# Performance work log

Hardware: AMD Instinct MI355X
Metric: run time of the kernel (lower is better)

## Reference

```python
import jax, jax.numpy as jnp
import numpy as np

ENC, STR_H, CELL_H, ATTN = 512, 256, 512, 512
B, L = 64, 1024


def setup_inputs() -> dict:
    key = jax.random.key(0)
    ks = jax.random.split(key, 12)
    s = lambda fan_in: 1.0 / np.sqrt(fan_in)
    return {
        "encoded_features_map": jax.random.normal(ks[0], (B, L, ENC), jnp.float32),
        "structural_hidden_state": jax.random.normal(ks[1], (1, B, STR_H), jnp.float32),
        "cell_content_hidden_state": jax.random.normal(ks[2], (1, B, CELL_H), jnp.float32),
        "W_enc": jax.random.uniform(ks[3], (ENC, ATTN), jnp.float32, -s(ENC), s(ENC)),
        "b_enc": jax.random.uniform(ks[4], (ATTN,), jnp.float32, -s(ENC), s(ENC)),
        "W_str": jax.random.uniform(ks[5], (STR_H, ATTN), jnp.float32, -s(STR_H), s(STR_H)),
        "b_str": jax.random.uniform(ks[6], (ATTN,), jnp.float32, -s(STR_H), s(STR_H)),
        "W_cell": jax.random.uniform(ks[7], (CELL_H, ATTN), jnp.float32, -s(CELL_H), s(CELL_H)),
        "b_cell": jax.random.uniform(ks[8], (ATTN,), jnp.float32, -s(CELL_H), s(CELL_H)),
        "W_comb": jax.random.uniform(ks[9], (ATTN, 1), jnp.float32, -s(ATTN), s(ATTN)),
        "b_comb": jax.random.uniform(ks[10], (1,), jnp.float32, -s(ATTN), s(ATTN)),
    }


def reference(encoded_features_map, structural_hidden_state, cell_content_hidden_state,
              W_enc, b_enc, W_str, b_str, W_cell, b_cell, W_comb, b_comb):
    # [B, L, A] projection of encoder features
    a_enc = jnp.einsum("ble,ea->bla", encoded_features_map, W_enc) + b_enc
    # [B, A] projections of the two hidden states (squeeze layer dim)
    a_str = structural_hidden_state[0] @ W_str + b_str
    a_cell = cell_content_hidden_state[0] @ W_cell + b_cell
    # broadcast add + ReLU + scalar score: [B, L]
    h = jax.nn.relu(a_enc + a_str[:, None, :] + a_cell[:, None, :])
    scores = jnp.einsum("bla,ao->bl", h, W_comb) + b_comb[0]
    weights = jax.nn.softmax(scores, axis=1)  # over sequence dim
    # weighted sum over L -> [B, ENC]
    context = jnp.einsum("bl,ble->be", weights, encoded_features_map)
    return context
```

## Files before the change

### kernel.cpp

```cpp
#include <hip/hip_runtime.h>
#include <stdint.h>

#define ENC_D 512
#define ATTN_D 512
#define STR_D 256
#define CELL_D 512
#define BATCH 64
#define SEQ 1024
#define NROWS (BATCH * SEQ)

typedef __bf16 bf16x8 __attribute__((ext_vector_type(8)));
typedef float f32x4 __attribute__((ext_vector_type(4)));

__device__ __forceinline__ unsigned short f2bf(float f) {
    unsigned int u = __float_as_uint(f);
    u += 0x7fffu + ((u >> 16) & 1u);
    return (unsigned short)(u >> 16);
}

__device__ __forceinline__ void lds_cp16(void* l, const void* g) {
    __builtin_amdgcn_global_load_lds(
        (const __attribute__((address_space(1))) unsigned int*)g,
        (__attribute__((address_space(3))) unsigned int*)l, 16, 0, 0);
}

__global__ __launch_bounds__(256) void k_prep_wt(const float* __restrict__ W,
                                                 unsigned short* __restrict__ WF) {
    __shared__ unsigned short T[64 * 68];
    const int t = threadIdx.x;
    const int ei = blockIdx.x >> 3, ni = blockIdx.x & 7;
    const int e0 = ei * 64, n0 = ni * 64;

#pragma unroll
    for (int i = 0; i < 4; ++i) {
        const int idx = t + i * 256;
        const int r = idx >> 4, c4 = idx & 15;
        const float4 v = *(const float4*)(W + (size_t)(e0 + r) * ATTN_D + n0 + c4 * 4);
        T[(c4 * 4 + 0) * 68 + r] = f2bf(v.x);
        T[(c4 * 4 + 1) * 68 + r] = f2bf(v.y);
        T[(c4 * 4 + 2) * 68 + r] = f2bf(v.z);
        T[(c4 * 4 + 3) * 68 + r] = f2bf(v.w);
    }
    __syncthreads();

#pragma unroll
    for (int i = 0; i < 2; ++i) {
        const int q = t + i * 256;
        const int n = q >> 3, ge = q & 7;
        union { unsigned short s[8]; uint4 u; } o;
#pragma unroll
        for (int j = 0; j < 8; ++j) o.s[j] = T[n * 68 + ge * 8 + j];
        const int ng = n0 + n;
        const int g = ei * 8 + ge;
        const int nt = ng >> 4, c = ng & 15;
        const int ks = g >> 2, quad = g & 3;
        const int gi = nt * 1024 + ks * 64 + quad * 16 + c;
        *(uint4*)(WF + (size_t)gi * 8) = o.u;
    }
}

__global__ __launch_bounds__(128) void k_bias_part(const float* __restrict__ str,
                                                   const float* __restrict__ cell,
                                                   const float* __restrict__ Wstr,
                                                   const float* __restrict__ Wcell,
                                                   float* __restrict__ part) {
    __shared__ float sj[64];
    const int jq = blockIdx.x, b = blockIdx.y, t = threadIdx.x;
    const float* hvec;
    const float* Wrow;
    if (jq < 4) { hvec = str + b * STR_D + jq * 64;            Wrow = Wstr + (size_t)(jq * 64) * ATTN_D; }
    else        { hvec = cell + b * CELL_D + (jq - 4) * 64;    Wrow = Wcell + (size_t)((jq - 4) * 64) * ATTN_D; }
    if (t < 64) sj[t] = hvec[t];
    __syncthreads();

    f32x4 acc = {0.f, 0.f, 0.f, 0.f};
#pragma unroll 8
    for (int i = 0; i < 64; ++i) {
        const float s = sj[i];
        const float4 wv = *(const float4*)(Wrow + (size_t)i * ATTN_D + t * 4);
        acc[0] += s * wv.x; acc[1] += s * wv.y; acc[2] += s * wv.z; acc[3] += s * wv.w;
    }
    *(f32x4*)(part + (size_t)(jq * BATCH + b) * ATTN_D + t * 4) = acc;
}

__global__ __launch_bounds__(256) void k_bias_fin(const float* __restrict__ part,
                                                  const float* __restrict__ b_enc,
                                                  const float* __restrict__ b_str,
                                                  const float* __restrict__ b_cell,
                                                  float* __restrict__ bias) {
    const int idx = blockIdx.x * 256 + threadIdx.x;
    const int b = idx >> 9, a = idx & 511;
    float s = b_enc[a] + b_str[a] + b_cell[a];
#pragma unroll
    for (int jq = 0; jq < 12; ++jq)
        s += part[(size_t)(jq * BATCH + b) * ATTN_D + a];
    bias[idx] = s;
}

__global__ __launch_bounds__(128, 2) void k_scores(const float* __restrict__ E,
                                                   const unsigned short* __restrict__ WF,
                                                   const float* __restrict__ bias,
                                                   const float* __restrict__ Wcomb,
                                                   float* __restrict__ scores) {
    __shared__ unsigned short buf[2][8192];

    const int tid = threadIdx.x;
    const int r0 = blockIdx.x * 64;
    const int b = blockIdx.x >> 4;
    const int w = tid >> 6, lane = tid & 63;
    const int quad = lane >> 4, c = lane & 15;

#pragma unroll
    for (int i = 0; i < 8; ++i)
        lds_cp16((char*)&buf[0][0] + i * 2048 + tid * 16,
                 (const char*)WF + i * 2048 + tid * 16);

    bf16x8 afr[2][16];
#pragma unroll
    for (int m = 0; m < 2; ++m) {
        const float* Ep = E + (size_t)(r0 + w * 32 + m * 16 + c) * ENC_D + quad * 8;
#pragma unroll
        for (int ks = 0; ks < 16; ++ks) {
            const float4 v0 = *(const float4*)(Ep + ks * 32);
            const float4 v1 = *(const float4*)(Ep + ks * 32 + 4);
            union { unsigned short s[8]; bf16x8 v; } u;
            u.s[0] = f2bf(v0.x); u.s[1] = f2bf(v0.y);
            u.s[2] = f2bf(v0.z); u.s[3] = f2bf(v0.w);
            u.s[4] = f2bf(v1.x); u.s[5] = f2bf(v1.y);
            u.s[6] = f2bf(v1.z); u.s[7] = f2bf(v1.w);
            afr[m][ks] = u.v;
        }
    }

    float sc0[4] = {0.f, 0.f, 0.f, 0.f};
    float sc1[4] = {0.f, 0.f, 0.f, 0.f};
    const float* biasb = bias + b * ATTN_D;

    __syncthreads();

    for (int ch = 0; ch < 32; ++ch) {
        if (ch < 31) {
            const char* gsrc = (const char*)WF + (size_t)(ch + 1) * 16384;
            char* ldst = (char*)&buf[(ch + 1) & 1][0];
#pragma unroll
            for (int i = 0; i < 8; ++i)
                lds_cp16(ldst + i * 2048 + tid * 16, gsrc + i * 2048 + tid * 16);
        }

        const unsigned short* wb = &buf[ch & 1][0];
        f32x4 a0 = {0.f, 0.f, 0.f, 0.f}, a1 = {0.f, 0.f, 0.f, 0.f};
#pragma unroll
        for (int ks = 0; ks < 16; ++ks) {
            const bf16x8 b0 = *(const bf16x8*)(wb + (ks * 64 + lane) * 8);
            a0 = __builtin_amdgcn_mfma_f32_16x16x32_bf16(afr[0][ks], b0, a0, 0, 0, 0);
            a1 = __builtin_amdgcn_mfma_f32_16x16x32_bf16(afr[1][ks], b0, a1, 0, 0, 0);
        }

        const int n = ch * 16 + c;
        const float bi = biasb[n], wc = Wcomb[n];
#pragma unroll
        for (int r = 0; r < 4; ++r) {
            float v;
            v = a0[r] + bi; sc0[r] += (v > 0.f ? v : 0.f) * wc;
            v = a1[r] + bi; sc1[r] += (v > 0.f ? v : 0.f) * wc;
        }
        __syncthreads();
    }

#pragma unroll
    for (int r = 0; r < 4; ++r) {
        float v0 = sc0[r], v1 = sc1[r];
        v0 += __shfl_xor(v0, 1); v1 += __shfl_xor(v1, 1);
        v0 += __shfl_xor(v0, 2); v1 += __shfl_xor(v1, 2);
        v0 += __shfl_xor(v0, 4); v1 += __shfl_xor(v1, 4);
        sc0[r] = v0 + __shfl_xor(v0, 8);
        sc1[r] = v1 + __shfl_xor(v1, 8);
    }
    if (c == 0) {
        const int g0 = r0 + w * 32 + quad * 4;
#pragma unroll
        for (int r = 0; r < 4; ++r) scores[g0 + r] = sc0[r];
#pragma unroll
        for (int r = 0; r < 4; ++r) scores[g0 + 16 + r] = sc1[r];
    }
}

__global__ __launch_bounds__(256) void k_softmax(float* __restrict__ s) {
    __shared__ float red[256];
    const int b = blockIdx.x, t = threadIdx.x;
    float v[4];
    float m = -1e30f;
#pragma unroll
    for (int i = 0; i < 4; ++i) {
        v[i] = s[b * SEQ + i * 256 + t];
        m = fmaxf(m, v[i]);
    }
    red[t] = m;
    __syncthreads();
    for (int o = 128; o > 0; o >>= 1) {
        if (t < o) red[t] = fmaxf(red[t], red[t + o]);
        __syncthreads();
    }
    m = red[0];
    __syncthreads();
    float sum = 0.f;
#pragma unroll
    for (int i = 0; i < 4; ++i) {
        v[i] = __expf(v[i] - m);
        sum += v[i];
    }
    red[t] = sum;
    __syncthreads();
    for (int o = 128; o > 0; o >>= 1) {
        if (t < o) red[t] += red[t + o];
        __syncthreads();
    }
    const float inv = 1.f / red[0];
#pragma unroll
    for (int i = 0; i < 4; ++i) s[b * SEQ + i * 256 + t] = v[i] * inv;
}

__global__ __launch_bounds__(128) void k_context(const float* __restrict__ E,
                                                 const float* __restrict__ wts,
                                                 float* __restrict__ part) {
    __shared__ float wl[64];
    const int blk = blockIdx.x, t = threadIdx.x;
    const int b = blk >> 4, lo = blk & 15;
    if (t < 64) wl[t] = wts[b * SEQ + lo * 64 + t];
    __syncthreads();
    const float* Ep = E + ((size_t)(b * SEQ + lo * 64)) * ENC_D + t * 4;
    f32x4 acc = {0.f, 0.f, 0.f, 0.f};
#pragma unroll 8
    for (int l = 0; l < 64; ++l) {
        const float4 v = *(const float4*)(Ep + (size_t)l * ENC_D);
        const float wv = wl[l];
        acc[0] += wv * v.x; acc[1] += wv * v.y;
        acc[2] += wv * v.z; acc[3] += wv * v.w;
    }
    *(f32x4*)(&part[(size_t)(b * 16 + lo) * ENC_D + t * 4]) = acc;
}

__global__ __launch_bounds__(256) void k_reduce(const float* __restrict__ part,
                                                float* __restrict__ out) {
    const int idx = blockIdx.x * 256 + threadIdx.x;
    const int b = idx >> 9, e = idx & 511;
    const float* p = part + (size_t)b * 16 * ENC_D + e;
    float s = 0.f;
#pragma unroll
    for (int i = 0; i < 16; ++i) s += p[i * ENC_D];
    out[idx] = s;
}

extern "C" void kernel_launch(void* const* d_in, const int* in_sizes, int n_in,
                              void* d_out, int out_size, void* d_ws, size_t ws_size,
                              hipStream_t stream) {
    const float* E      = (const float*)d_in[0];
    const float* str    = (const float*)d_in[1];
    const float* cell   = (const float*)d_in[2];
    const float* Wenc   = (const float*)d_in[3];
    const float* b_enc  = (const float*)d_in[4];
    const float* Wstr   = (const float*)d_in[5];
    const float* b_str  = (const float*)d_in[6];
    const float* Wcell  = (const float*)d_in[7];
    const float* b_cell = (const float*)d_in[8];
    const float* Wcomb  = (const float*)d_in[9];
    float* out = (float*)d_out;

    char* ws = (char*)d_ws;
    unsigned short* WF = (unsigned short*)ws;
    float* bias   = (float*)(ws + (512 << 10));
    float* scores = (float*)(ws + (512 << 10) + (128 << 10));
    float* part   = (float*)(ws + (512 << 10) + (128 << 10) + (256 << 10));
    float* bpart  = part;

    k_prep_wt<<<64, 256, 0, stream>>>(Wenc, WF);
    k_bias_part<<<dim3(12, 64), 128, 0, stream>>>(str, cell, Wstr, Wcell, bpart);
    k_bias_fin<<<128, 256, 0, stream>>>(bpart, b_enc, b_str, b_cell, bias);
    k_scores<<<NROWS / 64, 128, 0, stream>>>(E, WF, bias, Wcomb, scores);
    k_softmax<<<BATCH, 256, 0, stream>>>(scores);
    k_context<<<1024, 128, 0, stream>>>(E, scores, part);
    k_reduce<<<NROWS / 512, 256, 0, stream>>>(part, out);
}
```

Measured before the change: 288.3 us.

## Fuse prep, bias, softmax and reduction kernels into three launches

Merges weight conversion, bias partial products and output zeroing into one prep kernel, folds the bias finalisation into the scores kernel through LDS, and fuses softmax with the context weighted sum, using atomics to replace the separate reduce pass. The aim is to cut launch count and intermediate global round trips. The costs are a softmax recomputed redundantly by all 16 blocks of each batch, float atomics that make the output order-nondeterministic, and launch bounds on the scores kernel changed to one block per SIMD.

```diff
diff --git a/kernel.cpp b/kernel.cpp
--- a/kernel.cpp
+++ b/kernel.cpp
@@ -24,85 +24,91 @@
         (__attribute__((address_space(3))) unsigned int*)l, 16, 0, 0);
 }
 
-__global__ __launch_bounds__(256) void k_prep_wt(const float* __restrict__ W,
-                                                 unsigned short* __restrict__ WF) {
-    __shared__ unsigned short T[64 * 68];
-    const int t = threadIdx.x;
-    const int ei = blockIdx.x >> 3, ni = blockIdx.x & 7;
-    const int e0 = ei * 64, n0 = ni * 64;
-
-#pragma unroll
-    for (int i = 0; i < 4; ++i) {
-        const int idx = t + i * 256;
-        const int r = idx >> 4, c4 = idx & 15;
-        const float4 v = *(const float4*)(W + (size_t)(e0 + r) * ATTN_D + n0 + c4 * 4);
-        T[(c4 * 4 + 0) * 68 + r] = f2bf(v.x);
-        T[(c4 * 4 + 1) * 68 + r] = f2bf(v.y);
-        T[(c4 * 4 + 2) * 68 + r] = f2bf(v.z);
-        T[(c4 * 4 + 3) * 68 + r] = f2bf(v.w);
-    }
-    __syncthreads();
-
-#pragma unroll
-    for (int i = 0; i < 2; ++i) {
-        const int q = t + i * 256;
-        const int n = q >> 3, ge = q & 7;
-        union { unsigned short s[8]; uint4 u; } o;
-#pragma unroll
-        for (int j = 0; j < 8; ++j) o.s[j] = T[n * 68 + ge * 8 + j];
-        const int ng = n0 + n;
-        const int g = ei * 8 + ge;
-        const int nt = ng >> 4, c = ng & 15;
-        const int ks = g >> 2, quad = g & 3;
-        const int gi = nt * 1024 + ks * 64 + quad * 16 + c;
-        *(uint4*)(WF + (size_t)gi * 8) = o.u;
-    }
-}
-
-__global__ __launch_bounds__(128) void k_bias_part(const float* __restrict__ str,
-                                                   const float* __restrict__ cell,
-                                                   const float* __restrict__ Wstr,
-                                                   const float* __restrict__ Wcell,
-                                                   float* __restrict__ part) {
-    __shared__ float sj[64];
-    const int jq = blockIdx.x, b = blockIdx.y, t = threadIdx.x;
-    const float* hvec;
-    const float* Wrow;
-    if (jq < 4) { hvec = str + b * STR_D + jq * 64;            Wrow = Wstr + (size_t)(jq * 64) * ATTN_D; }
-    else        { hvec = cell + b * CELL_D + (jq - 4) * 64;    Wrow = Wcell + (size_t)((jq - 4) * 64) * ATTN_D; }
-    if (t < 64) sj[t] = hvec[t];
-    __syncthreads();
-
-    f32x4 acc = {0.f, 0.f, 0.f, 0.f};
+__global__ __launch_bounds__(256) void k_prep(const float* __restrict__ W,
+                                              unsigned short* __restrict__ WF,
+                                              const float* __restrict__ str,
+                                              const float* __restrict__ cell,
+                                              const float* __restrict__ Wstr,
+                                              const float* __restrict__ Wcell,
+                                              float* __restrict__ bpart,
+                                              float* __restrict__ outz) {
+    __shared__ char smraw[64 * 68 * 2];
+    const int bx = blockIdx.x, t = threadIdx.x;
+
+    if (bx < 64) {
+        unsigned short* T = (unsigned short*)smraw;
+        const int ei = bx >> 3, ni = bx & 7;
+        const int e0 = ei * 64, n0 = ni * 64;
+#pragma unroll
+        for (int i = 0; i < 4; ++i) {
+            const int idx = t + i * 256;
+            const int r = idx >> 4, c4 = idx & 15;
+            const float4 v = *(const float4*)(W + (size_t)(e0 + r) * ATTN_D + n0 + c4 * 4);
+            T[(c4 * 4 + 0) * 68 + r] = f2bf(v.x);
+            T[(c4 * 4 + 1) * 68 + r] = f2bf(v.y);
+            T[(c4 * 4 + 2) * 68 + r] = f2bf(v.z);
+            T[(c4 * 4 + 3) * 68 + r] = f2bf(v.w);
+        }
+        __syncthreads();
+#pragma unroll
+        for (int i = 0; i < 2; ++i) {
+            const int q = t + i * 256;
+            const int n = q >> 3, ge = q & 7;
+            union { unsigned short s[8]; uint4 u; } o;
+#pragma unroll
+            for (int j = 0; j < 8; ++j) o.s[j] = T[n * 68 + ge * 8 + j];
+            const int ng = n0 + n;
+            const int g = ei * 8 + ge;
+            const int nt = ng >> 4, c = ng & 15;
+            const int ks = g >> 2, quad = g & 3;
+            const int gi = nt * 1024 + ks * 64 + quad * 16 + c;
+            *(uint4*)(WF + (size_t)gi * 8) = o.u;
+        }
+    } else if (bx < 832) {
+        float* sj = (float*)smraw;
+        float* red = (float*)smraw + 64;
+        const int q = bx - 64;
+        const int b = q / 12, jq = q - b * 12;
+        const float* hvec;
+        const float* Wbase;
+        if (jq < 4) { hvec = str + b * STR_D + jq * 64;         Wbase = Wstr + (size_t)(jq * 64) * ATTN_D; }
+        else        { hvec = cell + b * CELL_D + (jq - 4) * 64; Wbase = Wcell + (size_t)((jq - 4) * 64) * ATTN_D; }
+        if (t < 64) sj[t] = hvec[t];
+        __syncthreads();
+        const int h = t >> 7, a4 = t & 127;
+        f32x4 acc = {0.f, 0.f, 0.f, 0.f};
 #pragma unroll 8
-    for (int i = 0; i < 64; ++i) {
-        const float s = sj[i];
-        const float4 wv = *(const float4*)(Wrow + (size_t)i * ATTN_D + t * 4);
-        acc[0] += s * wv.x; acc[1] += s * wv.y; acc[2] += s * wv.z; acc[3] += s * wv.w;
-    }
-    *(f32x4*)(part + (size_t)(jq * BATCH + b) * ATTN_D + t * 4) = acc;
-}
-
-__global__ __launch_bounds__(256) void k_bias_fin(const float* __restrict__ part,
-                                                  const float* __restrict__ b_enc,
-                                                  const float* __restrict__ b_str,
-                                                  const float* __restrict__ b_cell,
-                                                  float* __restrict__ bias) {
-    const int idx = blockIdx.x * 256 + threadIdx.x;
-    const int b = idx >> 9, a = idx & 511;
-    float s = b_enc[a] + b_str[a] + b_cell[a];
-#pragma unroll
-    for (int jq = 0; jq < 12; ++jq)
-        s += part[(size_t)(jq * BATCH + b) * ATTN_D + a];
-    bias[idx] = s;
-}
-
-__global__ __launch_bounds__(128, 2) void k_scores(const float* __restrict__ E,
+        for (int i = h * 32; i < h * 32 + 32; ++i) {
+            const float s = sj[i];
+            const float4 wv = *(const float4*)(Wbase + (size_t)i * ATTN_D + a4 * 4);
+            acc[0] += s * wv.x; acc[1] += s * wv.y; acc[2] += s * wv.z; acc[3] += s * wv.w;
+        }
+        if (h == 1) *(f32x4*)(red + a4 * 4) = acc;
+        __syncthreads();
+        if (h == 0) {
+            const f32x4 o = *(const f32x4*)(red + a4 * 4);
+            acc[0] += o[0]; acc[1] += o[1]; acc[2] += o[2]; acc[3] += o[3];
+            *(f32x4*)(bpart + (size_t)(jq * BATCH + b) * ATTN_D + a4 * 4) = acc;
+        }
+    } else {
+        const f32x4 z = {0.f, 0.f, 0.f, 0.f};
+        float* p = outz + (size_t)(bx - 832) * 2048 + t * 8;
+        *(f32x4*)p = z;
+        *(f32x4*)(p + 4) = z;
+    }
+}
+
+__global__ __launch_bounds__(128, 1) void k_scores(const float* __restrict__ E,
                                                    const unsigned short* __restrict__ WF,
-                                                   const float* __restrict__ bias,
+                                                   const float* __restrict__ bpart,
+                                                   const float* __restrict__ b_enc,
+                                                   const float* __restrict__ b_str,
+                                                   const float* __restrict__ b_cell,
                                                    const float* __restrict__ Wcomb,
                                                    float* __restrict__ scores) {
     __shared__ unsigned short buf[2][8192];
+    __shared__ float sbias[512];
+    __shared__ float sWc[512];
 
     const int tid = threadIdx.x;
     const int r0 = blockIdx.x * 64;
@@ -114,6 +120,25 @@
     for (int i = 0; i < 8; ++i)
         lds_cp16((char*)&buf[0][0] + i * 2048 + tid * 16,
                  (const char*)WF + i * 2048 + tid * 16);
+
+    {
+        const int a = tid * 4;
+        const float4 be = *(const float4*)(b_enc + a);
+        const float4 bs = *(const float4*)(b_str + a);
+        const float4 bc = *(const float4*)(b_cell + a);
+        f32x4 s;
+        s[0] = be.x + bs.x + bc.x; s[1] = be.y + bs.y + bc.y;
+        s[2] = be.z + bs.z + bc.z; s[3] = be.w + bs.w + bc.w;
+#pragma unroll
+        for (int jq = 0; jq < 12; ++jq) {
+            const float4 p = *(const float4*)(bpart + (size_t)(jq * BATCH + b) * ATTN_D + a);
+            s[0] += p.x; s[1] += p.y; s[2] += p.z; s[3] += p.w;
+        }
+        *(f32x4*)(sbias + a) = s;
+        const float4 wcv = *(const float4*)(Wcomb + a);
+        f32x4 wc4; wc4[0] = wcv.x; wc4[1] = wcv.y; wc4[2] = wcv.z; wc4[3] = wcv.w;
+        *(f32x4*)(sWc + a) = wc4;
+    }
 
     bf16x8 afr[2][16];
 #pragma unroll
@@ -134,7 +159,6 @@
 
     float sc0[4] = {0.f, 0.f, 0.f, 0.f};
     float sc1[4] = {0.f, 0.f, 0.f, 0.f};
-    const float* biasb = bias + b * ATTN_D;
 
     __syncthreads();
 
@@ -157,7 +181,7 @@
         }
 
         const int n = ch * 16 + c;
-        const float bi = biasb[n], wc = Wcomb[n];
+        const float bi = sbias[n], wc = sWc[n];
 #pragma unroll
         for (int r = 0; r < 4; ++r) {
             float v;
@@ -185,70 +209,54 @@
     }
 }
 
-__global__ __launch_bounds__(256) void k_softmax(float* __restrict__ s) {
-    __shared__ float red[256];
-    const int b = blockIdx.x, t = threadIdx.x;
-    float v[4];
-    float m = -1e30f;
-#pragma unroll
-    for (int i = 0; i < 4; ++i) {
-        v[i] = s[b * SEQ + i * 256 + t];
-        m = fmaxf(m, v[i]);
-    }
-    red[t] = m;
-    __syncthreads();
-    for (int o = 128; o > 0; o >>= 1) {
-        if (t < o) red[t] = fmaxf(red[t], red[t + o]);
-        __syncthreads();
-    }
-    m = red[0];
-    __syncthreads();
-    float sum = 0.f;
-#pragma unroll
-    for (int i = 0; i < 4; ++i) {
-        v[i] = __expf(v[i] - m);
-        sum += v[i];
-    }
-    red[t] = sum;
-    __syncthreads();
-    for (int o = 128; o > 0; o >>= 1) {
-        if (t < o) red[t] += red[t + o];
-        __syncthreads();
-    }
-    const float inv = 1.f / red[0];
-#pragma unroll
-    for (int i = 0; i < 4; ++i) s[b * SEQ + i * 256 + t] = v[i] * inv;
-}
-
-__global__ __launch_bounds__(128) void k_context(const float* __restrict__ E,
-                                                 const float* __restrict__ wts,
-                                                 float* __restrict__ part) {
-    __shared__ float wl[64];
+__global__ __launch_bounds__(128) void k_ctx(const float* __restrict__ E,
+                                             const float* __restrict__ scores,
+                                             float* __restrict__ out) {
+    __shared__ float ex[1024];
+    __shared__ float rtmp[4];
     const int blk = blockIdx.x, t = threadIdx.x;
     const int b = blk >> 4, lo = blk & 15;
-    if (t < 64) wl[t] = wts[b * SEQ + lo * 64 + t];
+
+    float v[8];
+    float m = -1e30f;
+#pragma unroll
+    for (int i = 0; i < 8; ++i) {
+        v[i] = scores[b * SEQ + i * 128 + t];
+        m = fmaxf(m, v[i]);
+    }
+#pragma unroll
+    for (int o = 32; o > 0; o >>= 1) m = fmaxf(m, __shfl_xor(m, o));
+    if ((t & 63) == 0) rtmp[t >> 6] = m;
     __syncthreads();
-    const float* Ep = E + ((size_t)(b * SEQ + lo * 64)) * ENC_D + t * 4;
+    m = fmaxf(rtmp[0], rtmp[1]);
+
+    float s = 0.f;
+#pragma unroll
+    for (int i = 0; i < 8; ++i) {
+        const float e = __expf(v[i] - m);
+        ex[i * 128 + t] = e;
+        s += e;
+    }
+#pragma unroll
+    for (int o = 32; o > 0; o >>= 1) s += __shfl_xor(s, o);
+    if ((t & 63) == 0) rtmp[2 + (t >> 6)] = s;
+    __syncthreads();
+    const float inv = 1.f / (rtmp[2] + rtmp[3]);
+
+    const float* Ep = E + (size_t)(b * SEQ + lo * 64) * ENC_D + t * 4;
     f32x4 acc = {0.f, 0.f, 0.f, 0.f};
 #pragma unroll 8
     for (int l = 0; l < 64; ++l) {
-        const float4 v = *(const float4*)(Ep + (size_t)l * ENC_D);
-        const float wv = wl[l];
-        acc[0] += wv * v.x; acc[1] += wv * v.y;
-        acc[2] += wv * v.z; acc[3] += wv * v.w;
-    }
-    *(f32x4*)(&part[(size_t)(b * 16 + lo) * ENC_D + t * 4]) = acc;
-}
-
-__global__ __launch_bounds__(256) void k_reduce(const float* __restrict__ part,
-                                                float* __restrict__ out) {
-    const int idx = blockIdx.x * 256 + threadIdx.x;
-    const int b = idx >> 9, e = idx & 511;
-    const float* p = part + (size_t)b * 16 * ENC_D + e;
-    float s = 0.f;
-#pragma unroll
-    for (int i = 0; i < 16; ++i) s += p[i * ENC_D];
-    out[idx] = s;
+        const float4 e4 = *(const float4*)(Ep + (size_t)l * ENC_D);
+        const float wv = ex[lo * 64 + l];
+        acc[0] += wv * e4.x; acc[1] += wv * e4.y;
+        acc[2] += wv * e4.z; acc[3] += wv * e4.w;
+    }
+    float* op = out + b * ENC_D + t * 4;
+    atomicAdd(op + 0, acc[0] * inv);
+    atomicAdd(op + 1, acc[1] * inv);
+    atomicAdd(op + 2, acc[2] * inv);
+    atomicAdd(op + 3, acc[3] * inv);
 }
 
 extern "C" void kernel_launch(void* const* d_in, const int* in_sizes, int n_in,
@@ -259,25 +267,23 @@
     const float* cell   = (const float*)d_in[2];
     const float* Wenc   = (const float*)d_in[3];
     const float* b_enc  = (const float*)d_in[4];
+    const float* b_str  = (const float*)d_in[5];
+    const float* Wcell  = (const float*)d_in[7];
     const float* Wstr   = (const float*)d_in[5];
-    const float* b_str  = (const float*)d_in[6];
-    const float* Wcell  = (const float*)d_in[7];
-    const float* b_cell = (const float*)d_in[8];
+    const float* Wstr_  = (const float*)d_in[5];
+    const float* bstr_  = (const float*)d_in[6];
+    const float* Wcell_ = (const float*)d_in[7];
+    const float* bcell_ = (const float*)d_in[8];
     const float* Wcomb  = (const float*)d_in[9];
     float* out = (float*)d_out;
 
     char* ws = (char*)d_ws;
     unsigned short* WF = (unsigned short*)ws;
-    float* bias   = (float*)(ws + (512 << 10));
-    float* scores = (float*)(ws + (512 << 10) + (128 << 10));
-    float* part   = (float*)(ws + (512 << 10) + (128 << 10) + (256 << 10));
-    float* bpart  = part;
-
-    k_prep_wt<<<64, 256, 0, stream>>>(Wenc, WF);
-    k_bias_part<<<dim3(12, 64), 128, 0, stream>>>(str, cell, Wstr, Wcell, bpart);
-    k_bias_fin<<<128, 256, 0, stream>>>(bpart, b_enc, b_str, b_cell, bias);
-    k_scores<<<NROWS / 64, 128, 0, stream>>>(E, WF, bias, Wcomb, scores);
-    k_softmax<<<BATCH, 256, 0, stream>>>(scores);
-    k_context<<<1024, 128, 0, stream>>>(E, scores, part);
-    k_reduce<<<NROWS / 512, 256, 0, stream>>>(part, out);
-}
+    float* scores = (float*)(ws + (512 << 10));
+    float* bpart  = (float*)(ws + (512 << 10) + (256 << 10));
+
+    k_prep<<<848, 256, 0, stream>>>(Wenc, WF, str, cell, Wstr_, Wcell_, bpart, out);
+    k_scores<<<NROWS / 64, 128, 0, stream>>>(E, WF, bpart, b_enc, bstr_, bcell_, Wcomb, scores);
+    k_ctx<<<1024, 128, 0, stream>>>(E, scores, out);
+    (void)Wstr; (void)Wcell; (void)b_str;
+}
```

Result: slower. 298.8 us (+3.6%).
